# Performance work log

Measured on AMD Instinct MI355X. Metric: run time of the kernel, lower is better.

Reference implementation:

```python
import jax, jax.numpy as jnp
import numpy as np

D_MODEL = 768
N_HEADS = 12
D_K = 768
D_V = 768
SEQ = 2048
BATCH = 2


def setup_inputs() -> dict:
    key = jax.random.key(0)
    ks = jax.random.split(key, 9)
    s = 0.02
    return {
        "x": jax.random.normal(ks[0], (SEQ, BATCH, D_MODEL), dtype=jnp.float32),
        "Wq": jax.random.normal(ks[1], (D_MODEL, D_K), dtype=jnp.float32) * s,
        "bq": jnp.zeros((D_K,), dtype=jnp.float32),
        "Wk": jax.random.normal(ks[2], (D_MODEL, D_K), dtype=jnp.float32) * s,
        "bk": jnp.zeros((D_K,), dtype=jnp.float32),
        "Wv": jax.random.normal(ks[3], (D_MODEL, D_V), dtype=jnp.float32) * s,
        "bv": jnp.zeros((D_V,), dtype=jnp.float32),
        "Wo": jax.random.normal(ks[4], (D_V, D_MODEL), dtype=jnp.float32) * s,
        "bo": jnp.zeros((D_MODEL,), dtype=jnp.float32),
    }


def reference(x, Wq, bq, Wk, bk, Wv, bv, Wo, bo):
    # x: (S, B, D)
    S, B, D = x.shape
    H = N_HEADS
    hk = D_K // H
    hv = D_V // H
    q = (x @ Wq + bq).reshape(S, B, H, hk)
    k = (x @ Wk + bk).reshape(S, B, H, hk)
    v = (x @ Wv + bv).reshape(S, B, H, hv)
    scale = 1.0 / np.sqrt(hk).astype(np.float32)
    # scores: (B, H, S_q, S_k)
    att = jnp.einsum("sbhd,tbhd->bhst", q, k) * scale
    causal = jnp.triu(jnp.ones((S, S), dtype=bool), k=1)  # True above diagonal
    att = jnp.where(causal, jnp.float32(-jnp.inf), att)
    att = jax.nn.softmax(att, axis=-1)
    y = jnp.einsum("bhst,tbhd->sbhd", att, v).reshape(S, B, D_V)
    return y @ Wo + bo  # (S, B, D)
```

## Files before the change

kernel.cpp:

```cpp
#include <hip/hip_runtime.h>

typedef __attribute__((ext_vector_type(8))) short short8;
typedef __attribute__((ext_vector_type(4))) short s16x4;
typedef __attribute__((ext_vector_type(4))) float f32x4;

#define NHEADS 12
#define SEQLEN 2048
#define HEADD  64
#define DMODEL 768

__device__ __forceinline__ short cvtbf(float f) {
  unsigned u = __builtin_bit_cast(unsigned, f);
  u += 0x7fffu + ((u >> 16) & 1u);
  return (short)(u >> 16);
}

__device__ __forceinline__ void gload16(const void* g, void* l) {
  __builtin_amdgcn_global_load_lds((const __attribute__((address_space(1))) void*)g,
                                   (__attribute__((address_space(3))) void*)l, 16, 0, 0);
}

__device__ __forceinline__ void ds_write_hi16(short* p, float v) {
  asm volatile("ds_write_b16_d16_hi %0, %1"
               : : "v"((__attribute__((address_space(3))) short*)p), "v"(v) : "memory");
}

__global__ void prep_kernel(const float* __restrict__ x, short* __restrict__ xb,
                            const float* __restrict__ w0, const float* __restrict__ w1,
                            const float* __restrict__ w2, const float* __restrict__ w3,
                            short* __restrict__ wt, short* __restrict__ wot) {
  __shared__ float t[32][33];
  const int tid = threadIdx.x;
  if (blockIdx.x < 1536) {
    int i = blockIdx.x * 256 + tid;
    const float* p = x + (size_t)i * 8;
    short8 v;
#pragma unroll
    for (int j = 0; j < 8; ++j) v[j] = cvtbf(p[j]);
    *(short8*)(xb + (size_t)i * 8) = v;
    return;
  }
  int bx = blockIdx.x - 1536;
  int bz = bx / 576, rem = bx - bz * 576;
  int bxx = rem % 24, byy = rem / 24;
  const float* W = bz == 0 ? w0 : bz == 1 ? w1 : bz == 2 ? w2 : w3;
  short* O = bz < 3 ? wt + (size_t)bz * (768 * 768) : wot;
  int tx = tid & 31, ty = tid >> 5;
  int n0 = bxx * 32, k0 = byy * 32;
#pragma unroll
  for (int j = 0; j < 4; ++j)
    t[ty + j * 8][tx] = W[(k0 + ty + j * 8) * 768 + n0 + tx];
  __syncthreads();
#pragma unroll
  for (int j = 0; j < 4; ++j)
    O[(n0 + ty + j * 8) * 768 + k0 + tx] = cvtbf(t[tx][ty + j * 8]);
}

template <bool DBUF>
__device__ __forceinline__ void gemm_core128(const short* __restrict__ A,
                                             const short* __restrict__ Bt,
                                             short* sA, short* sB,
                                             int bm, int bn, f32x4 acc[4][4]) {
  const int tid = threadIdx.x;
  const int w = tid >> 6, lane = tid & 63;
  const int quad = lane >> 4, l16 = lane & 15;
  const int wm = (w & 1) * 64, wn = (w >> 1) * 64;

  int gA[4], gB[4], lbase[4];
#pragma unroll
  for (int j = 0; j < 4; ++j) {
    int slot = j * 256 + w * 64 + lane;
    int r = slot >> 3, c = (slot & 7) ^ (r & 7);
    gA[j] = (bm * 128 + r) * 768 + c * 8;
    gB[j] = (bn * 128 + r) * 768 + c * 8;
    lbase[j] = (j * 256 + w * 64) * 8;
  }

  if (DBUF) {
#pragma unroll
    for (int j = 0; j < 4; ++j) {
      gload16(A + gA[j], sA + lbase[j]);
      gload16(Bt + gB[j], sB + lbase[j]);
    }
    int pb = 0;
    for (int kt = 0; kt < 12; ++kt) {
      __syncthreads();
      if (kt + 1 < 12) {
        int o = (pb ^ 1) * 8192;
#pragma unroll
        for (int j = 0; j < 4; ++j) {
          gload16(A + gA[j] + (kt + 1) * 64, sA + o + lbase[j]);
          gload16(Bt + gB[j] + (kt + 1) * 64, sB + o + lbase[j]);
        }
      }
      const short* pa = sA + pb * 8192;
      const short* pbv = sB + pb * 8192;
#pragma unroll
      for (int ks = 0; ks < 2; ++ks) {
        int cp = (ks * 4 + quad) ^ (l16 & 7);
        short8 a[4], b[4];
#pragma unroll
        for (int mt = 0; mt < 4; ++mt)
          a[mt] = *(const short8*)(pa + (wm + mt * 16 + l16) * 64 + cp * 8);
#pragma unroll
        for (int nt = 0; nt < 4; ++nt)
          b[nt] = *(const short8*)(pbv + (wn + nt * 16 + l16) * 64 + cp * 8);
#pragma unroll
        for (int mt = 0; mt < 4; ++mt)
#pragma unroll
          for (int nt = 0; nt < 4; ++nt)
            acc[mt][nt] = __builtin_amdgcn_mfma_f32_16x16x32_bf16(a[mt], b[nt], acc[mt][nt], 0, 0, 0);
      }
      pb ^= 1;
    }
  } else {
    for (int kt = 0; kt < 12; ++kt) {
      __syncthreads();
#pragma unroll
      for (int j = 0; j < 4; ++j) {
        gload16(A + gA[j] + kt * 64, sA + lbase[j]);
        gload16(Bt + gB[j] + kt * 64, sB + lbase[j]);
      }
      __syncthreads();
#pragma unroll
      for (int ks = 0; ks < 2; ++ks) {
        int cp = (ks * 4 + quad) ^ (l16 & 7);
        short8 a[4], b[4];
#pragma unroll
        for (int mt = 0; mt < 4; ++mt)
          a[mt] = *(const short8*)(sA + (wm + mt * 16 + l16) * 64 + cp * 8);
#pragma unroll
        for (int nt = 0; nt < 4; ++nt)
          b[nt] = *(const short8*)(sB + (wn + nt * 16 + l16) * 64 + cp * 8);
#pragma unroll
        for (int mt = 0; mt < 4; ++mt)
#pragma unroll
          for (int nt = 0; nt < 4; ++nt)
            acc[mt][nt] = __builtin_amdgcn_mfma_f32_16x16x32_bf16(a[mt], b[nt], acc[mt][nt], 0, 0, 0);
      }
    }
  }
}

__global__ __launch_bounds__(256, 3) void qkv_gemm(
    const short* __restrict__ A, const short* __restrict__ Bt,
    const float* __restrict__ bq, const float* __restrict__ bk, const float* __restrict__ bv,
    short* __restrict__ oq, short* __restrict__ ok, short* __restrict__ ov) {
  __shared__ short sAB[2 * 128 * 64];
  f32x4 acc[4][4];
  const f32x4 z4 = {0.f, 0.f, 0.f, 0.f};
#pragma unroll
  for (int mt = 0; mt < 4; ++mt)
#pragma unroll
    for (int nt = 0; nt < 4; ++nt) acc[mt][nt] = z4;

  const int bm = blockIdx.x, bn = blockIdx.y;
  gemm_core128<false>(A, Bt, sAB, sAB + 8192, bm, bn, acc);

  const int seg = bn / 6, bn_l = bn % 6;
  const float* bias = seg == 0 ? bq : seg == 1 ? bk : bv;
  short* outp = seg == 0 ? oq : seg == 1 ? ok : ov;

  const int tid = threadIdx.x;
  const int w = tid >> 6, lane = tid & 63;
  const int quad = lane >> 4, l16 = lane & 15;
  const int wm = (w & 1) * 64, wn = (w >> 1) * 64;

  __syncthreads();

  if (seg < 2) {
#pragma unroll
    for (int nt = 0; nt < 4; ++nt) {
      int n = wn + nt * 16 + l16;
      float bval = bias[bn_l * 128 + n];
      int c = n >> 3, nl = n & 7;
#pragma unroll
      for (int mt = 0; mt < 4; ++mt) {
#pragma unroll
        for (int r = 0; r < 4; ++r) {
          int m = wm + mt * 16 + quad * 4 + r;
          float v = acc[mt][nt][r] + bval;
          if (seg == 0) v *= 0.1803368801f;
          sAB[m * 128 + ((c ^ (m & 7)) << 3) + nl] = cvtbf(v);
        }
      }
    }
  } else {
#pragma unroll
    for (int nt = 0; nt < 4; ++nt) {
      int n = wn + nt * 16 + l16;
      float bval = bias[bn_l * 128 + n];
#pragma unroll
      for (int mt = 0; mt < 4; ++mt) {
#pragma unroll
        for (int r = 0; r < 4; ++r) {
          int m = wm + mt * 16 + quad * 4 + r;
          int mm = ((m & 1) << 6) | (m >> 1);
          float v = acc[mt][nt][r] + bval;
          sAB[n * 128 + (((mm >> 3) ^ (n & 7)) << 3) + (mm & 7)] = cvtbf(v);
        }
      }
    }
  }
  __syncthreads();

  if (seg < 2) {
#pragma unroll
    for (int j = 0; j < 8; ++j) {
      int ch = j * 256 + tid;
      int m = ch >> 4, c = ch & 15;
      short8 v = *(const short8*)(sAB + m * 128 + ((c ^ (m & 7)) << 3));
      int mg = bm * 128 + m;
      int s = mg >> 1, b = mg & 1;
      int h = bn_l * 2 + (c >> 3), d0 = (c & 7) * 8;
      *(short8*)(outp + (((size_t)(b * NHEADS + h) * SEQLEN + s) * HEADD + d0)) = v;
    }
  } else {
#pragma unroll
    for (int j = 0; j < 8; ++j) {
      int ch = j * 256 + tid;
      int n = ch >> 4, c = ch & 15;
      short8 v = *(const short8*)(sAB + n * 128 + ((c ^ (n & 7)) << 3));
      int b = c >> 3, s0 = bm * 64 + (c & 7) * 8;
      int h = bn_l * 2 + (n >> 6), d = n & 63;
      *(short8*)(outp + (((size_t)(b * NHEADS + h) * HEADD + d) * SEQLEN + s0)) = v;
    }
  }
}

#define AE(qi, ts, nt) ((qi) | ((ts) << 8) | ((nt) << 16))
__device__ const int ATTN_TAB[80] = {
  AE(31,0,8), AE(31,8,8), AE(31,16,8), AE(31,24,8),
  AE(30,0,8), AE(30,8,8), AE(30,16,8),
  AE(29,0,8), AE(29,8,8), AE(29,16,8),
  AE(28,0,8), AE(28,8,8), AE(28,16,8),
  AE(27,0,8), AE(27,8,8), AE(27,16,8),
  AE(26,0,8), AE(26,8,8), AE(26,16,8),
  AE(25,0,8), AE(25,8,8), AE(25,16,8),
  AE(24,0,8), AE(24,8,8), AE(24,16,8),
  AE(23,0,8), AE(23,8,8), AE(23,16,8),
  AE(22,0,8), AE(22,8,8),
  AE(21,0,8), AE(21,8,8),
  AE(20,0,8), AE(20,8,8),
  AE(19,0,8), AE(19,8,8),
  AE(18,0,8), AE(18,8,8),
  AE(17,0,8), AE(17,8,8),
  AE(16,0,8), AE(16,8,8),
  AE(15,0,8), AE(15,8,8),
  AE(14,0,8), AE(13,0,8), AE(12,0,8), AE(11,0,8),
  AE(10,0,8), AE(9,0,8),  AE(8,0,8),  AE(7,0,8),
  AE(30,24,7), AE(22,16,7), AE(14,8,7), AE(6,0,7),
  AE(29,24,6), AE(21,16,6), AE(13,8,6), AE(5,0,6),
  AE(28,24,5), AE(20,16,5), AE(12,8,5), AE(4,0,5),
  AE(27,24,4), AE(19,16,4), AE(11,8,4), AE(3,0,4),
  AE(26,24,3), AE(18,16,3), AE(10,8,3), AE(2,0,3),
  AE(25,24,2), AE(17,16,2), AE(9,8,2),  AE(1,0,2),
  AE(24,24,1), AE(16,16,1), AE(8,8,1),  AE(0,0,1),
};
__device__ const int PBASE[32] = {
  0,0,0,0,0,0,0,0,
  0,2,4,6,8,10,12,14,
  16,19,22,25,28,31,34,37,
  40,44,48,52,56,60,64,68};

__global__ __launch_bounds__(256, 4) void attn_kernel(
    const short* __restrict__ Q, const short* __restrict__ K,
    const short* __restrict__ Vt, short* __restrict__ Y,
    float* __restrict__ Of, float* __restrict__ lf) {
  __shared__ short sK[2][64 * 64];
  __shared__ short sV[2][64 * 64];
  __shared__ short sP[64 * 64];
  const int tid = threadIdx.x;
  const int w = tid >> 6, lane = tid & 63;
  const int quad = lane >> 4, l16 = lane & 15;
  const int e = ATTN_TAB[blockIdx.x / 24];
  const int bh = blockIdx.x % 24;
  const int qi = e & 255, ts = (e >> 8) & 255, ntl = e >> 16;
  const int q0 = qi << 6;
  const short* Qb = Q + (size_t)bh * (SEQLEN * HEADD);
  const short* Kb = K + (size_t)bh * (SEQLEN * HEADD);
  const short* Vb = Vt + (size_t)bh * (SEQLEN * HEADD);

  short8 aq[2];
#pragma unroll
  for (int ks = 0; ks < 2; ++ks)
    aq[ks] = *(const short8*)(Qb + (q0 + w * 16 + l16) * 64 + ks * 32 + quad * 8);

  const short8 bones = {0x3F80, 0x3F80, 0x3F80, 0x3F80, 0x3F80, 0x3F80, 0x3F80, 0x3F80};
  f32x4 acc_o[4], acc_l;
  const f32x4 z4 = {0.f, 0.f, 0.f, 0.f};
#pragma unroll
  for (int nt = 0; nt < 4; ++nt) acc_o[nt] = z4;
  acc_l = z4;

  int gK[2], gV[2], lbase[2];
#pragma unroll
  for (int j = 0; j < 2; ++j) {
    int slot = j * 256 + w * 64 + lane;
    int r = slot >> 3, c = (slot & 7) ^ (r & 7);
    gK[j] = r * 64 + c * 8;
    gV[j] = r * 2048 + c * 8;
    lbase[j] = (j * 256 + w * 64) * 8;
  }

  const int qrow = q0 + w * 16 + quad * 4;
  const int tend = ts + ntl;

#pragma unroll
  for (int j = 0; j < 2; ++j) {
    gload16(Kb + (ts << 6) * 64 + gK[j], &sK[0][lbase[j]]);
    gload16(Vb + (ts << 6) + gV[j], &sV[0][lbase[j]]);
  }

  int pb = 0;
  for (int it = ts; it < tend; ++it) {
    __syncthreads();
    if (it + 1 < tend) {
      const int t1 = (it + 1) << 6;
#pragma unroll
      for (int j = 0; j < 2; ++j) {
        gload16(Kb + t1 * 64 + gK[j], &sK[pb ^ 1][lbase[j]]);
        gload16(Vb + t1 + gV[j], &sV[pb ^ 1][lbase[j]]);
      }
    }
    const short* sk = sK[pb];
    const short* sv = sV[pb];

    f32x4 sc[4];
#pragma unroll
    for (int nt = 0; nt < 4; ++nt) sc[nt] = z4;
#pragma unroll
    for (int ks = 0; ks < 2; ++ks) {
      int cp = (ks * 4 + quad) ^ (l16 & 7);
#pragma unroll
      for (int nt = 0; nt < 4; ++nt) {
        short8 bk = *(const short8*)(sk + (nt * 16 + l16) * 64 + cp * 8);
        sc[nt] = __builtin_amdgcn_mfma_f32_16x16x32_bf16(aq[ks], bk, sc[nt], 0, 0, 0);
      }
    }

    if (it == qi) {
      const int t0 = it << 6;
#pragma unroll
      for (int nt = 0; nt < 4; ++nt)
#pragma unroll
        for (int r = 0; r < 4; ++r) {
          int t = t0 + nt * 16 + l16;
          if (t > qrow + r) sc[nt][r] = -1e30f;
        }
    }

#pragma unroll
    for (int nt = 0; nt < 4; ++nt)
#pragma unroll
      for (int r = 0; r < 4; ++r) {
        float p = __builtin_amdgcn_exp2f(sc[nt][r]);
        int rq = w * 16 + quad * 4 + r;
        int t = nt * 16 + l16;
        int c = t >> 3;
        ds_write_hi16(&sP[rq * 64 + ((c ^ (rq & 7)) * 8 + (t & 7))], p);
      }

#pragma unroll
    for (int kst = 0; kst < 2; ++kst) {
      int rq = w * 16 + l16;
      int cpa = (kst * 4 + quad) ^ (rq & 7);
      short8 ap = *(const short8*)(sP + rq * 64 + cpa * 8);
      acc_l = __builtin_amdgcn_mfma_f32_16x16x32_bf16(ap, bones, acc_l, 0, 0, 0);
#pragma unroll
      for (int nt = 0; nt < 4; ++nt) {
        int row = nt * 16 + l16;
        int cv = (kst * 4 + quad) ^ (row & 7);
        short8 bv = *(const short8*)(sv + row * 64 + cv * 8);
        acc_o[nt] = __builtin_amdgcn_mfma_f32_16x16x32_bf16(ap, bv, acc_o[nt], 0, 0, 0);
      }
    }
    pb ^= 1;
  }

  if (qi < 8) {
    const int b = bh / NHEADS, h = bh % NHEADS;
#pragma unroll
    for (int r = 0; r < 4; ++r) {
      float rl = __builtin_amdgcn_rcpf(acc_l[r]);
      int srow = q0 + w * 16 + quad * 4 + r;
#pragma unroll
      for (int nt = 0; nt < 4; ++nt)
        Y[(srow * 2 + b) * DMODEL + h * 64 + nt * 16 + l16] = cvtbf(acc_o[nt][r] * rl);
    }
  } else {
    const int slot = bh * 72 + PBASE[qi] + (ts >> 3);
    float* Ob = Of + (size_t)slot * 4096;
#pragma unroll
    for (int r = 0; r < 4; ++r) {
      int row = w * 16 + quad * 4 + r;
#pragma unroll
      for (int nt = 0; nt < 4; ++nt)
        Ob[row * 64 + nt * 16 + l16] = acc_o[nt][r];
      if (l16 == 0) lf[slot * 64 + row] = acc_l[r];
    }
  }
}

__global__ void attn_merge(const float* __restrict__ Of, const float* __restrict__ lf,
                           short* __restrict__ Y) {
  const int bh = blockIdx.x % 24, qi = 8 + blockIdx.x / 24;
  const int nch = (qi >> 3) + 1;
  const int base = bh * 72 + PBASE[qi];
  const float* O0 = Of + (size_t)base * 4096;
  const float* L0 = lf + base * 64;
  const int b = bh / NHEADS, h = bh % NHEADS;
  const int tid = threadIdx.x;
#pragma unroll
  for (int j = 0; j < 4; ++j) {
    int i4 = j * 256 + tid;
    int row = i4 >> 4, col4 = (i4 & 15) * 4;
    f32x4 o = *(const f32x4*)(O0 + (size_t)i4 * 4);
    float l = L0[row];
    for (int c = 1; c < nch; ++c) {
      o += *(const f32x4*)(O0 + (size_t)c * 4096 + (size_t)i4 * 4);
      l += L0[c * 64 + row];
    }
    float rl = __builtin_amdgcn_rcpf(l);
    s16x4 y;
#pragma unroll
    for (int k = 0; k < 4; ++k) y[k] = cvtbf(o[k] * rl);
    int srow = qi * 64 + row;
    *(s16x4*)(Y + (size_t)(srow * 2 + b) * DMODEL + h * 64 + col4) = y;
  }
}

__global__ __launch_bounds__(256, 2) void oproj_gemm(
    const short* __restrict__ A, const short* __restrict__ Bt,
    const float* __restrict__ bo, float* __restrict__ out) {
  __shared__ short sA[2 * 128 * 64];
  __shared__ short sB[2 * 128 * 64];
  f32x4 acc[4][4];
  const f32x4 z4 = {0.f, 0.f, 0.f, 0.f};
#pragma unroll
  for (int mt = 0; mt < 4; ++mt)
#pragma unroll
    for (int nt = 0; nt < 4; ++nt) acc[mt][nt] = z4;

  const int bm = blockIdx.x, bn = blockIdx.y;
  gemm_core128<true>(A, Bt, sA, sB, bm, bn, acc);

  const int tid = threadIdx.x;
  const int w = tid >> 6, lane = tid & 63;
  const int quad = lane >> 4, l16 = lane & 15;
  const int wm = (w & 1) * 64, wn = (w >> 1) * 64;

#pragma unroll
  for (int nt = 0; nt < 4; ++nt) {
    int n = bn * 128 + wn + nt * 16 + l16;
    float bval = bo[n];
#pragma unroll
    for (int mt = 0; mt < 4; ++mt) {
      int rowb = wm + mt * 16 + quad * 4;
#pragma unroll
      for (int r = 0; r < 4; ++r) {
        int m = bm * 128 + rowb + r;
        out[(size_t)m * 768 + n] = acc[mt][nt][r] + bval;
      }
    }
  }
}

extern "C" void kernel_launch(void* const* d_in, const int* in_sizes, int n_in,
                              void* d_out, int out_size, void* d_ws, size_t ws_size,
                              hipStream_t stream) {
  const float* x  = (const float*)d_in[0];
  const float* Wq = (const float*)d_in[1];
  const float* bq = (const float*)d_in[2];
  const float* Wk = (const float*)d_in[3];
  const float* bk = (const float*)d_in[4];
  const float* Wv = (const float*)d_in[5];
  const float* bv = (const float*)d_in[6];
  const float* Wo = (const float*)d_in[7];
  const float* bo = (const float*)d_in[8];
  float* out = (float*)d_out;

  short* ws  = (short*)d_ws;
  short* xb  = ws;
  short* wt  = ws + 3145728;
  short* wot = ws + 4915200;
  short* qw  = ws + 5505024;
  short* kw  = ws + 8650752;
  short* vw  = ws + 11796480;
  short* yw  = ws + 14942208;
  float* Of  = (float*)(ws + 18087936);
  float* lf  = Of + 7077888;

  prep_kernel<<<3840, 256, 0, stream>>>(x, xb, Wq, Wk, Wv, Wo, wt, wot);
  qkv_gemm<<<dim3(32, 18), 256, 0, stream>>>(xb, wt, bq, bk, bv, qw, kw, vw);
  attn_kernel<<<1920, 256, 0, stream>>>(qw, kw, vw, yw, Of, lf);
  attn_merge<<<576, 256, 0, stream>>>(Of, lf, yw);
  oproj_gemm<<<dim3(32, 6), 256, 0, stream>>>(yw, wot, bo, out);
}
```

Measured before the change: 149.3 us.

## Fuse split-KV merge into attention kernel via last-arriver atomic counter

After: 425.3 us. +184.9%, slower.

```diff
diff --git a/kernel.cpp b/kernel.cpp
--- a/kernel.cpp
+++ b/kernel.cpp
@@ -266,7 +266,7 @@
 __global__ __launch_bounds__(256, 4) void attn_kernel(
     const short* __restrict__ Q, const short* __restrict__ K,
     const short* __restrict__ Vt, short* __restrict__ Y,
-    float* __restrict__ Of, float* __restrict__ lf) {
+    float* __restrict__ Of, float* __restrict__ lf, unsigned* __restrict__ cnt) {
   __shared__ short sK[2][64 * 64];
   __shared__ short sV[2][64 * 64];
   __shared__ short sP[64 * 64];
@@ -378,8 +378,9 @@
     pb ^= 1;
   }
 
+  const int b = bh / NHEADS, h = bh % NHEADS;
+
   if (qi < 8) {
-    const int b = bh / NHEADS, h = bh % NHEADS;
 #pragma unroll
     for (int r = 0; r < 4; ++r) {
       float rl = __builtin_amdgcn_rcpf(acc_l[r]);
@@ -388,45 +389,51 @@
       for (int nt = 0; nt < 4; ++nt)
         Y[(srow * 2 + b) * DMODEL + h * 64 + nt * 16 + l16] = cvtbf(acc_o[nt][r] * rl);
     }
-  } else {
-    const int slot = bh * 72 + PBASE[qi] + (ts >> 3);
-    float* Ob = Of + (size_t)slot * 4096;
-#pragma unroll
-    for (int r = 0; r < 4; ++r) {
-      int row = w * 16 + quad * 4 + r;
-#pragma unroll
-      for (int nt = 0; nt < 4; ++nt)
-        Ob[row * 64 + nt * 16 + l16] = acc_o[nt][r];
-      if (l16 == 0) lf[slot * 64 + row] = acc_l[r];
-    }
-  }
-}
-
-__global__ void attn_merge(const float* __restrict__ Of, const float* __restrict__ lf,
-                           short* __restrict__ Y) {
-  const int bh = blockIdx.x % 24, qi = 8 + blockIdx.x / 24;
+    return;
+  }
+
   const int nch = (qi >> 3) + 1;
+  const int ci = ts >> 3;
   const int base = bh * 72 + PBASE[qi];
+  const int slot = base + ci;
+  float* Ob = Of + (size_t)slot * 4096;
+#pragma unroll
+  for (int r = 0; r < 4; ++r) {
+    int row = w * 16 + quad * 4 + r;
+#pragma unroll
+    for (int nt = 0; nt < 4; ++nt)
+      Ob[row * 64 + nt * 16 + l16] = acc_o[nt][r];
+    if (l16 == 0) lf[slot * 64 + row] = acc_l[r];
+  }
+
+  __threadfence();
+  __syncthreads();
+  volatile int* flag = (volatile int*)sP;
+  if (tid == 0) {
+    unsigned old = atomicAdd(&cnt[bh * 24 + (qi - 8)], 1u);
+    *flag = (old == (unsigned)(nch - 1));
+  }
+  __syncthreads();
+  if (!*flag) return;
+  __threadfence();
+
   const float* O0 = Of + (size_t)base * 4096;
   const float* L0 = lf + base * 64;
-  const int b = bh / NHEADS, h = bh % NHEADS;
-  const int tid = threadIdx.x;
-#pragma unroll
-  for (int j = 0; j < 4; ++j) {
-    int i4 = j * 256 + tid;
-    int row = i4 >> 4, col4 = (i4 & 15) * 4;
-    f32x4 o = *(const f32x4*)(O0 + (size_t)i4 * 4);
-    float l = L0[row];
-    for (int c = 1; c < nch; ++c) {
-      o += *(const f32x4*)(O0 + (size_t)c * 4096 + (size_t)i4 * 4);
-      l += L0[c * 64 + row];
-    }
+#pragma unroll
+  for (int r = 0; r < 4; ++r) {
+    int row = w * 16 + quad * 4 + r;
+    float l = acc_l[r];
+    for (int c = 0; c < nch; ++c)
+      if (c != ci) l += L0[c * 64 + row];
     float rl = __builtin_amdgcn_rcpf(l);
-    s16x4 y;
-#pragma unroll
-    for (int k = 0; k < 4; ++k) y[k] = cvtbf(o[k] * rl);
-    int srow = qi * 64 + row;
-    *(s16x4*)(Y + (size_t)(srow * 2 + b) * DMODEL + h * 64 + col4) = y;
+    int srow = q0 + row;
+#pragma unroll
+    for (int nt = 0; nt < 4; ++nt) {
+      float o = acc_o[nt][r];
+      for (int c = 0; c < nch; ++c)
+        if (c != ci) o += O0[(size_t)c * 4096 + row * 64 + nt * 16 + l16];
+      Y[(srow * 2 + b) * DMODEL + h * 64 + nt * 16 + l16] = cvtbf(o * rl);
+    }
   }
 }
 
@@ -490,10 +497,11 @@
   short* yw  = ws + 14942208;
   float* Of  = (float*)(ws + 18087936);
   float* lf  = Of + 7077888;
-
+  unsigned* cnt = (unsigned*)(lf + 110592);
+
+  hipMemsetAsync(cnt, 0, 576 * sizeof(unsigned), stream);
   prep_kernel<<<3840, 256, 0, stream>>>(x, xb, Wq, Wk, Wv, Wo, wt, wot);
   qkv_gemm<<<dim3(32, 18), 256, 0, stream>>>(xb, wt, bq, bk, bv, qw, kw, vw);
-  attn_kernel<<<1920, 256, 0, stream>>>(qw, kw, vw, yw, Of, lf);
-  attn_merge<<<576, 256, 0, stream>>>(Of, lf, yw);
+  attn_kernel<<<1920, 256, 0, stream>>>(qw, kw, vw, yw, Of, lf, cnt);
   oproj_gemm<<<dim3(32, 6), 256, 0, stream>>>(yw, wot, bo, out);
 }
```
